# Kernel optimization log

Hardware: AMD Instinct MI355X
Metric: run time of the kernel (lower is better)

The kernel has to match this reference:

```python
import math
import jax, jax.numpy as jnp
import numpy as np

N_REP = 4      # n_heads / n_kv_heads
DIM = 4096     # n_heads * head_dim
NEG_INF = -1e9 # additive mask value for disallowed positions


def setup_inputs() -> dict:
    key = jax.random.key(0)
    k0, k1, k2 = jax.random.split(key, 3)
    B, S, H, KVH, D, MAX_S = 2, 2048, 32, 8, 128, 2048
    q = jax.random.normal(k0, (B, S, H, D), dtype=jnp.float32)
    k = jax.random.normal(k1, (B, KVH, S, D), dtype=jnp.float32)
    v = jax.random.normal(k2, (B, KVH, S, D), dtype=jnp.float32)
    cache_k = jnp.zeros((B, KVH, MAX_S, D), dtype=jnp.float32)
    cache_v = jnp.zeros((B, KVH, MAX_S, D), dtype=jnp.float32)
    # full causal additive mask, indexed by input_pos rows in forward
    causal = jnp.tril(jnp.ones((MAX_S, MAX_S), dtype=bool))
    mask = jnp.where(causal, 0.0, NEG_INF).astype(jnp.float32)
    input_pos = jnp.arange(S, dtype=jnp.int32)
    return {
        "input_pos": input_pos,
        "q": q,
        "k": k,
        "v": v,
        "bsz": B,
        "seqlen": S,
        "mask": mask,
        "cache_k": cache_k,
        "cache_v": cache_v,
    }


def reference(input_pos, q, k, v, bsz, seqlen, mask, cache_k, cache_v):
    # q: (b, s, H, d) -> (b, H, s, d)
    qh = jnp.transpose(q, (0, 2, 1, 3))
    # KV cache update: write k, v at input_pos, return full cache (b, KVH, MAX_S, d)
    ck = cache_k.at[:, :, input_pos, :].set(k)
    cv = cache_v.at[:, :, input_pos, :].set(v)
    # GQA: repeat each kv head n_rep times -> (b, H, MAX_S, d)
    kf = jnp.repeat(ck, N_REP, axis=1)
    vf = jnp.repeat(cv, N_REP, axis=1)
    scale = 1.0 / math.sqrt(qh.shape[-1])
    attn_mask = mask[input_pos]  # (s, MAX_S)
    # scores: (b, H, s, MAX_S)
    attn = jnp.einsum("bhsd,bhtd->bhst", qh, kf) * scale + attn_mask
    w = jax.nn.softmax(attn, axis=-1)
    y = jnp.einsum("bhst,bhtd->bhsd", w, vf)
    # (b, H, s, d) -> (b, s, H*d)
    return jnp.transpose(y, (0, 2, 1, 3)).reshape(bsz, seqlen, DIM)
```

## Files before the change

### kernel.cpp

```cpp
#include <hip/hip_runtime.h>
#include <hip/hip_bf16.h>

typedef __attribute__((ext_vector_type(8))) short bf16x8;
typedef __attribute__((ext_vector_type(4))) float f32x4;
typedef __attribute__((ext_vector_type(8))) float f32x8;
typedef __attribute__((ext_vector_type(2))) float f32x2;
typedef __attribute__((ext_vector_type(8))) __bf16 bfv8;
typedef __attribute__((ext_vector_type(4))) __bf16 bfv4;
typedef __attribute__((ext_vector_type(2))) __bf16 bfv2;
typedef __attribute__((ext_vector_type(2))) unsigned int u32x2;

#define B_ 2
#define S_ 2048
#define H_ 32
#define KVH_ 8
#define D_ 128
#define BM 128
#define BN 64
#define NQT (S_ / BM)

__device__ __forceinline__ bf16x8 cvt8(f32x8 v) {
    union { bfv8 b; bf16x8 s; } u;
    u.b = __builtin_convertvector(v, bfv8);
    return u.s;
}

#define GLD16(g, l) __builtin_amdgcn_global_load_lds(                     \
    (const __attribute__((address_space(1))) unsigned int*)(g),           \
    (__attribute__((address_space(3))) unsigned int*)(l), 16, 0, 0)

__global__ __launch_bounds__(256) void conv_k(const float* __restrict__ k,
                                              short* __restrict__ kws) {
    const int idx = (blockIdx.x * 256 + threadIdx.x) * 8;
    f32x8 a = *(const f32x8*)(k + idx);
    *(bf16x8*)(kws + idx) = cvt8(a);
}

__global__ __launch_bounds__(256) void conv_vt(const float* __restrict__ v,
                                               short* __restrict__ vws) {
    __shared__ short tl[64 * 68];
    const int d0 = blockIdx.x * 64;
    const int t0 = blockIdx.y * 64;
    const int z  = blockIdx.z;
    const int tid = threadIdx.x;
    const float* vb = v + (size_t)z * S_ * D_;
    short* wb = vws + (size_t)z * D_ * S_;
    #pragma unroll
    for (int i = 0; i < 4; ++i) {
        const int chunk = i * 256 + tid;
        const int tr = chunk >> 4;
        const int c4 = (chunk & 15) << 2;
        float4 f = *(const float4*)(vb + (t0 + tr) * D_ + d0 + c4);
        union { bfv4 b; ushort4 s; } u;
        u.b = __builtin_convertvector((f32x4){f.x, f.y, f.z, f.w}, bfv4);
        *(ushort4*)(&tl[tr * 68 + c4]) = u.s;
    }
    __syncthreads();
    #pragma unroll
    for (int i = 0; i < 2; ++i) {
        const int chunk = i * 256 + tid;
        const int d = chunk >> 3;
        const int u8 = chunk & 7;
        bf16x8 r;
        #pragma unroll
        for (int w = 0; w < 8; ++w) {
            const int t = 2 * u8 + (w >> 2) + 16 * (w & 3);
            r[w] = tl[t * 68 + d];
        }
        *(bf16x8*)(wb + (size_t)(d0 + d) * S_ + t0 + u8 * 8) = r;
    }
}

#define STAGE(ti_, bufi_)  do {                                            \
    const short* kt2_ = kt + (ti_) * (BN * D_);                            \
    const short* vt2_ = vt + (ti_) * BN;                                   \
    short* kdst_ = &lds_k[bufi_][0];                                       \
    short* vdst_ = &lds_v[bufi_][0];                                       \
    _Pragma("unroll")                                                      \
    for (int rd_ = 0; rd_ < 4; ++rd_) {                                    \
        const int slot_ = rd_ * 256 + tid;                                 \
        const int r_  = slot_ >> 4;                                        \
        const int cg_ = (slot_ & 15) ^ (r_ & 7);                           \
        GLD16(kt2_ + r_ * D_ + cg_ * 8, kdst_ + (rd_ * 256 + wave * 64) * 8); \
    }                                                                      \
    _Pragma("unroll")                                                      \
    for (int rd_ = 0; rd_ < 4; ++rd_) {                                    \
        const int slot_ = rd_ * 256 + tid;                                 \
        const int d_  = slot_ >> 3;                                        \
        const int cg_ = (slot_ & 7) ^ (d_ & 7);                            \
        GLD16(vt2_ + (size_t)d_ * S_ + cg_ * 8, vdst_ + (rd_ * 256 + wave * 64) * 8); \
    }                                                                      \
} while (0)

__global__ __launch_bounds__(256, 2) void fa_fwd(
    const float* __restrict__ q, const short* __restrict__ kws,
    const short* __restrict__ vws, float* __restrict__ out)
{
    __shared__ short lds_k[2][64 * 128];
    __shared__ short lds_v[2][128 * 64];
    __shared__ short lds_p[4 * 32 * 64];

    const int flat = blockIdx.x + NQT * (blockIdx.y + H_ * blockIdx.z);
    const int xcd  = flat & 7;
    const int idx  = flat >> 3;
    const int work = xcd * 128 + idx;
    const int bkvh = work >> 6;
    const int rem  = work & 63;
    const int qt   = (NQT - 1) - (rem >> 2);
    const int b    = bkvh >> 3;
    const int kvh  = bkvh & 7;
    const int h    = (kvh << 2) | (rem & 3);

    const int tid  = threadIdx.x;
    const int wave = __builtin_amdgcn_readfirstlane(tid >> 6);
    const int lane = tid & 63;
    const int quad = lane >> 4;
    const int l16  = lane & 15;
    const int x7   = l16 & 7;
    const int s0   = qt * BM;
    const int wr   = s0 + wave * 32;

    const float sl2e = 0.08838834764831843f * 1.4426950408889634f;

    const short* kt = kws + (size_t)(b * KVH_ + kvh) * S_ * D_;
    const short* vt = vws + (size_t)(b * KVH_ + kvh) * D_ * S_;
    short* pw = lds_p + wave * 2048;

    const int nt = 2 * qt + 2;

    STAGE(0, 0);

    bf16x8 qf[2][4];
    #pragma unroll
    for (int mb = 0; mb < 2; ++mb) {
        const float* qrow = q + (size_t)((b * S_ + wr + mb * 16 + l16) * H_ + h) * D_;
        #pragma unroll
        for (int c = 0; c < 4; ++c) {
            f32x8 a = *(const f32x8*)(qrow + c * 32 + quad * 8);
            qf[mb][c] = cvt8(a * sl2e);
        }
    }

    f32x4 o[2][8];
    #pragma unroll
    for (int mb = 0; mb < 2; ++mb)
        #pragma unroll
        for (int db = 0; db < 8; ++db) o[mb][db] = (f32x4){0.f, 0.f, 0.f, 0.f};
    float Lr[2][4] = {{0.f,0.f,0.f,0.f},{0.f,0.f,0.f,0.f}};

    int bi = 0;
    for (int ti = 0; ti < nt; ++ti) {
        if (ti + 1 < nt) {
            STAGE(ti + 1, bi ^ 1);
            asm volatile("s_waitcnt vmcnt(8)" ::: "memory");
        } else {
            asm volatile("s_waitcnt vmcnt(0)" ::: "memory");
        }
        __builtin_amdgcn_s_barrier();
        __builtin_amdgcn_sched_barrier(0);

        const int t0 = ti * BN;
        if (t0 <= wr + 31) {
            const short* kb = &lds_k[bi][0];
            const short* vb = &lds_v[bi][0];

            f32x4 sc[2][4];
            #pragma unroll
            for (int mb = 0; mb < 2; ++mb)
                #pragma unroll
                for (int nb = 0; nb < 4; ++nb) sc[mb][nb] = (f32x4){0.f,0.f,0.f,0.f};
            __builtin_amdgcn_s_setprio(1);
            #pragma unroll
            for (int c = 0; c < 4; ++c) {
                #pragma unroll
                for (int nb = 0; nb < 4; ++nb) {
                    bf16x8 kf = *(const bf16x8*)(&kb[(nb * 16 + l16) * 128 +
                                                     (((c * 4 + quad) ^ x7) * 8)]);
                    sc[0][nb] = __builtin_amdgcn_mfma_f32_16x16x32_bf16(qf[0][c], kf, sc[0][nb], 0, 0, 0);
                    sc[1][nb] = __builtin_amdgcn_mfma_f32_16x16x32_bf16(qf[1][c], kf, sc[1][nb], 0, 0, 0);
                }
            }
            __builtin_amdgcn_s_setprio(0);

            const bool needmask = (t0 + BN - 1 > wr);
            if (needmask) {
                #pragma unroll
                for (int mb = 0; mb < 2; ++mb)
                    #pragma unroll
                    for (int nb = 0; nb < 4; ++nb)
                        #pragma unroll
                        for (int r = 0; r < 4; ++r) {
                            const int tcol = t0 + nb * 16 + l16;
                            const int srow = wr + mb * 16 + quad * 4 + r;
                            if (tcol > srow) sc[mb][nb][r] = -1e30f;
                        }
            }
            #pragma unroll
            for (int mb = 0; mb < 2; ++mb)
                #pragma unroll
                for (int nb = 0; nb < 4; ++nb)
                    #pragma unroll
                    for (int r = 0; r < 4; ++r)
                        sc[mb][nb][r] = exp2f(sc[mb][nb][r]);
            #pragma unroll
            for (int mb = 0; mb < 2; ++mb)
                #pragma unroll
                for (int r = 0; r < 4; ++r)
                    Lr[mb][r] += (sc[mb][0][r] + sc[mb][1][r]) + (sc[mb][2][r] + sc[mb][3][r]);

            #pragma unroll
            for (int mb = 0; mb < 2; ++mb)
                #pragma unroll
                for (int r = 0; r < 4; ++r) {
                    const int mw = mb * 16 + quad * 4 + r;
                    union { bfv2 b; unsigned u; } p0, p1;
                    p0.b = __builtin_convertvector((f32x2){sc[mb][0][r], sc[mb][1][r]}, bfv2);
                    p1.b = __builtin_convertvector((f32x2){sc[mb][2][r], sc[mb][3][r]}, bfv2);
                    *(u32x2*)(&pw[mw * 64 + (((l16 >> 1) ^ (mw & 7)) * 8) + (l16 & 1) * 4]) =
                        (u32x2){p0.u, p1.u};
                }

            bf16x8 pf[2][2];
            #pragma unroll
            for (int mb = 0; mb < 2; ++mb)
                #pragma unroll
                for (int kk = 0; kk < 2; ++kk)
                    pf[mb][kk] = *(const bf16x8*)(&pw[(mb * 16 + l16) * 64 +
                                                     (((kk * 4 + quad) ^ x7) * 8)]);
            __builtin_amdgcn_s_setprio(1);
            #pragma unroll
            for (int kk = 0; kk < 2; ++kk) {
                #pragma unroll
                for (int db = 0; db < 8; ++db) {
                    bf16x8 vf = *(const bf16x8*)(&vb[(db * 16 + l16) * 64 +
                                                     (((kk * 4 + quad) ^ x7) * 8)]);
                    o[0][db] = __builtin_amdgcn_mfma_f32_16x16x32_bf16(pf[0][kk], vf, o[0][db], 0, 0, 0);
                    o[1][db] = __builtin_amdgcn_mfma_f32_16x16x32_bf16(pf[1][kk], vf, o[1][db], 0, 0, 0);
                }
            }
            __builtin_amdgcn_s_setprio(0);
        }

        __builtin_amdgcn_s_barrier();
        __builtin_amdgcn_sched_barrier(0);
        bi ^= 1;
    }

    #pragma unroll
    for (int mb = 0; mb < 2; ++mb)
        #pragma unroll
        for (int r = 0; r < 4; ++r) {
            float l = Lr[mb][r];
            l += __shfl_xor(l, 1, 16);
            l += __shfl_xor(l, 2, 16);
            l += __shfl_xor(l, 4, 16);
            l += __shfl_xor(l, 8, 16);
            Lr[mb][r] = 1.0f / l;
        }
    #pragma unroll
    for (int mb = 0; mb < 2; ++mb)
        #pragma unroll
        for (int r = 0; r < 4; ++r) {
            const int srow = wr + mb * 16 + quad * 4 + r;
            float* orow = out + (size_t)(b * S_ + srow) * (H_ * D_) + h * D_;
            #pragma unroll
            for (int db = 0; db < 8; ++db)
                orow[db * 16 + l16] = o[mb][db][r] * Lr[mb][r];
        }
}

extern "C" void kernel_launch(void* const* d_in, const int* in_sizes, int n_in,
                              void* d_out, int out_size, void* d_ws, size_t ws_size,
                              hipStream_t stream) {
    const float* q = (const float*)d_in[1];
    const float* k = (const float*)d_in[2];
    const float* v = (const float*)d_in[3];
    float* out = (float*)d_out;
    short* kws = (short*)d_ws;
    short* vws = kws + (size_t)B_ * KVH_ * S_ * D_;

    conv_k<<<(B_ * KVH_ * S_ * D_) / (256 * 8), 256, 0, stream>>>(k, kws);
    conv_vt<<<dim3(D_ / 64, S_ / 64, B_ * KVH_), 256, 0, stream>>>(v, vws);
    fa_fwd<<<dim3(NQT, H_, B_), 256, 0, stream>>>(q, kws, vws, out);
}
```

Baseline: 258.1 us.

## Drop K/V double buffering and raise occupancy to four blocks per CU

```diff
diff --git a/kernel.cpp b/kernel.cpp
--- a/kernel.cpp
+++ b/kernel.cpp
@@ -71,34 +71,32 @@
     }
 }
 
-#define STAGE(ti_, bufi_)  do {                                            \
+#define STAGE(ti_)  do {                                                   \
     const short* kt2_ = kt + (ti_) * (BN * D_);                            \
     const short* vt2_ = vt + (ti_) * BN;                                   \
-    short* kdst_ = &lds_k[bufi_][0];                                       \
-    short* vdst_ = &lds_v[bufi_][0];                                       \
     _Pragma("unroll")                                                      \
     for (int rd_ = 0; rd_ < 4; ++rd_) {                                    \
         const int slot_ = rd_ * 256 + tid;                                 \
         const int r_  = slot_ >> 4;                                        \
         const int cg_ = (slot_ & 15) ^ (r_ & 7);                           \
-        GLD16(kt2_ + r_ * D_ + cg_ * 8, kdst_ + (rd_ * 256 + wave * 64) * 8); \
+        GLD16(kt2_ + r_ * D_ + cg_ * 8, lds_k + (rd_ * 256 + wave * 64) * 8); \
     }                                                                      \
     _Pragma("unroll")                                                      \
     for (int rd_ = 0; rd_ < 4; ++rd_) {                                    \
         const int slot_ = rd_ * 256 + tid;                                 \
         const int d_  = slot_ >> 3;                                        \
         const int cg_ = (slot_ & 7) ^ (d_ & 7);                            \
-        GLD16(vt2_ + (size_t)d_ * S_ + cg_ * 8, vdst_ + (rd_ * 256 + wave * 64) * 8); \
+        GLD16(vt2_ + (size_t)d_ * S_ + cg_ * 8, lds_v + (rd_ * 256 + wave * 64) * 8); \
     }                                                                      \
 } while (0)
 
-__global__ __launch_bounds__(256, 2) void fa_fwd(
+__global__ __launch_bounds__(256, 4) void fa_fwd(
     const float* __restrict__ q, const short* __restrict__ kws,
     const short* __restrict__ vws, float* __restrict__ out)
 {
-    __shared__ short lds_k[2][64 * 128];
-    __shared__ short lds_v[2][128 * 64];
-    __shared__ short lds_p[4 * 32 * 64];
+    __shared__ short lds_k[64 * 128];
+    __shared__ short lds_v[128 * 64];
+    __shared__ short lds_p[4 * 16 * 64];
 
     const int flat = blockIdx.x + NQT * (blockIdx.y + H_ * blockIdx.z);
     const int xcd  = flat & 7;
@@ -124,11 +122,11 @@
 
     const short* kt = kws + (size_t)(b * KVH_ + kvh) * S_ * D_;
     const short* vt = vws + (size_t)(b * KVH_ + kvh) * D_ * S_;
-    short* pw = lds_p + wave * 2048;
+    short* pw = lds_p + wave * 1024;
 
     const int nt = 2 * qt + 2;
 
-    STAGE(0, 0);
+    STAGE(0);
 
     bf16x8 qf[2][4];
     #pragma unroll
@@ -148,22 +146,13 @@
         for (int db = 0; db < 8; ++db) o[mb][db] = (f32x4){0.f, 0.f, 0.f, 0.f};
     float Lr[2][4] = {{0.f,0.f,0.f,0.f},{0.f,0.f,0.f,0.f}};
 
-    int bi = 0;
     for (int ti = 0; ti < nt; ++ti) {
-        if (ti + 1 < nt) {
-            STAGE(ti + 1, bi ^ 1);
-            asm volatile("s_waitcnt vmcnt(8)" ::: "memory");
-        } else {
-            asm volatile("s_waitcnt vmcnt(0)" ::: "memory");
-        }
+        asm volatile("s_waitcnt vmcnt(0)" ::: "memory");
         __builtin_amdgcn_s_barrier();
         __builtin_amdgcn_sched_barrier(0);
 
         const int t0 = ti * BN;
         if (t0 <= wr + 31) {
-            const short* kb = &lds_k[bi][0];
-            const short* vb = &lds_v[bi][0];
-
             f32x4 sc[2][4];
             #pragma unroll
             for (int mb = 0; mb < 2; ++mb)
@@ -174,8 +163,8 @@
             for (int c = 0; c < 4; ++c) {
                 #pragma unroll
                 for (int nb = 0; nb < 4; ++nb) {
-                    bf16x8 kf = *(const bf16x8*)(&kb[(nb * 16 + l16) * 128 +
-                                                     (((c * 4 + quad) ^ x7) * 8)]);
+                    bf16x8 kf = *(const bf16x8*)(&lds_k[(nb * 16 + l16) * 128 +
+                                                        (((c * 4 + quad) ^ x7) * 8)]);
                     sc[0][nb] = __builtin_amdgcn_mfma_f32_16x16x32_bf16(qf[0][c], kf, sc[0][nb], 0, 0, 0);
                     sc[1][nb] = __builtin_amdgcn_mfma_f32_16x16x32_bf16(qf[1][c], kf, sc[1][nb], 0, 0, 0);
                 }
@@ -209,41 +198,38 @@
                     Lr[mb][r] += (sc[mb][0][r] + sc[mb][1][r]) + (sc[mb][2][r] + sc[mb][3][r]);
 
             #pragma unroll
-            for (int mb = 0; mb < 2; ++mb)
+            for (int mb = 0; mb < 2; ++mb) {
                 #pragma unroll
                 for (int r = 0; r < 4; ++r) {
-                    const int mw = mb * 16 + quad * 4 + r;
+                    const int rw = quad * 4 + r;
                     union { bfv2 b; unsigned u; } p0, p1;
                     p0.b = __builtin_convertvector((f32x2){sc[mb][0][r], sc[mb][1][r]}, bfv2);
                     p1.b = __builtin_convertvector((f32x2){sc[mb][2][r], sc[mb][3][r]}, bfv2);
-                    *(u32x2*)(&pw[mw * 64 + (((l16 >> 1) ^ (mw & 7)) * 8) + (l16 & 1) * 4]) =
+                    *(u32x2*)(&pw[rw * 64 + (((l16 >> 1) ^ (rw & 7)) * 8) + (l16 & 1) * 4]) =
                         (u32x2){p0.u, p1.u};
                 }
-
-            bf16x8 pf[2][2];
-            #pragma unroll
-            for (int mb = 0; mb < 2; ++mb)
+                bf16x8 pf[2];
                 #pragma unroll
                 for (int kk = 0; kk < 2; ++kk)
-                    pf[mb][kk] = *(const bf16x8*)(&pw[(mb * 16 + l16) * 64 +
-                                                     (((kk * 4 + quad) ^ x7) * 8)]);
-            __builtin_amdgcn_s_setprio(1);
-            #pragma unroll
-            for (int kk = 0; kk < 2; ++kk) {
-                #pragma unroll
-                for (int db = 0; db < 8; ++db) {
-                    bf16x8 vf = *(const bf16x8*)(&vb[(db * 16 + l16) * 64 +
-                                                     (((kk * 4 + quad) ^ x7) * 8)]);
-                    o[0][db] = __builtin_amdgcn_mfma_f32_16x16x32_bf16(pf[0][kk], vf, o[0][db], 0, 0, 0);
-                    o[1][db] = __builtin_amdgcn_mfma_f32_16x16x32_bf16(pf[1][kk], vf, o[1][db], 0, 0, 0);
+                    pf[kk] = *(const bf16x8*)(&pw[l16 * 64 +
+                                                  (((kk * 4 + quad) ^ x7) * 8)]);
+                __builtin_amdgcn_s_setprio(1);
+                #pragma unroll
+                for (int kk = 0; kk < 2; ++kk) {
+                    #pragma unroll
+                    for (int db = 0; db < 8; ++db) {
+                        bf16x8 vf = *(const bf16x8*)(&lds_v[(db * 16 + l16) * 64 +
+                                                            (((kk * 4 + quad) ^ x7) * 8)]);
+                        o[mb][db] = __builtin_amdgcn_mfma_f32_16x16x32_bf16(pf[kk], vf, o[mb][db], 0, 0, 0);
+                    }
                 }
+                __builtin_amdgcn_s_setprio(0);
             }
-            __builtin_amdgcn_s_setprio(0);
         }
 
         __builtin_amdgcn_s_barrier();
         __builtin_amdgcn_sched_barrier(0);
-        bi ^= 1;
+        if (ti + 1 < nt) STAGE(ti + 1);
     }
 
     #pragma unroll
```

Result: slower. 713.1 us (+176.3%).
